# Kernel optimization log

Measured on AMD Instinct MI355X. Metric: run time of the kernel, lower is better.

The kernel has to match this reference:

```python
import jax, jax.numpy as jnp
import numpy as np

COMMITMENT_COST = 0.25


def setup_inputs() -> dict:
    key = jax.random.key(0)
    k1, k2 = jax.random.split(key)
    B, D, H, W = 16, 256, 32, 32
    K = 8192
    z = jax.random.normal(k1, (B, D, H, W), dtype=jnp.float32)
    embeddings = jax.random.uniform(k2, (K, D), dtype=jnp.float32,
                                    minval=-1.0 / K, maxval=1.0 / K)
    return {"z": z, "embeddings": embeddings}


def reference(z, embeddings):
    B, D, H, W = z.shape
    # NCHW -> NHWC, flatten spatial+batch to code vectors [N, D]
    z_p = jnp.transpose(z, (0, 2, 3, 1))
    z_flat = z_p.reshape(-1, D)
    # squared-distance via matmul: ||z||^2 + ||e||^2 - 2 z.e^T  -> [N, K]
    d = (jnp.sum(z_flat * z_flat, axis=1, keepdims=True)
         + jnp.sum(embeddings * embeddings, axis=1)
         - 2.0 * jnp.matmul(z_flat, embeddings.T))
    encoding_indices = jnp.argmin(d, axis=1)  # [N]
    quantized = embeddings[encoding_indices].reshape(z_p.shape)  # [B,H,W,D]
    e_latent_loss = jnp.mean((jax.lax.stop_gradient(quantized) - z_p) ** 2)
    q_latent_loss = jnp.mean((quantized - jax.lax.stop_gradient(z_p)) ** 2)
    loss = q_latent_loss + COMMITMENT_COST * e_latent_loss
    # straight-through estimator
    quantized_st = z_p + jax.lax.stop_gradient(quantized - z_p)
    out = jnp.transpose(quantized_st, (0, 3, 1, 2))  # back to NCHW
    return out, loss, encoding_indices.reshape(B, H, W)
```

## Files before the change

kernel.cpp:

```cpp
#include <hip/hip_runtime.h>

#define B_    16
#define D_    256
#define H_    32
#define W_    32
#define SP    1024
#define N_TOT 16384
#define K_    8192
#define ZB    (D_*SP)

#define BIAS_  0.03125f
#define DELTA_ 2.5e-4f

typedef __attribute__((ext_vector_type(8))) short bf16x8;
typedef __attribute__((ext_vector_type(4))) short bf16x4;
typedef __attribute__((ext_vector_type(4))) float f32x4;

#define GLOAD_LDS16(g, l) \
    __builtin_amdgcn_global_load_lds((const __attribute__((address_space(1))) void*)(g), \
                                     (__attribute__((address_space(3))) void*)(l), 16, 0, 0)

__device__ __forceinline__ unsigned short f2bf(float f) {
    unsigned u = __float_as_uint(f);
    u += 0x7FFFu + ((u >> 16) & 1u);
    return (unsigned short)(u >> 16);
}

__device__ __forceinline__ void merge2(unsigned &a1, unsigned &a2,
                                       unsigned b1, unsigned b2) {
    unsigned m1  = min(a1, b1);
    unsigned hi  = max(a1, b1);
    unsigned sel = (a1 < b1) ? a2 : b2;
    a2 = min(hi, sel);
    a1 = m1;
}


__global__ __launch_bounds__(256)
void cvt_e_enorm(const float* __restrict__ emb, short* __restrict__ ET3,
                 float* __restrict__ enorm, float* __restrict__ enormB) {
    int t = threadIdx.x;
    int k = blockIdx.x * 4 + (t >> 6);
    int l = t & 63;
    float4 v = *(const float4*)(emb + (size_t)k * D_ + l * 4);
    float sum = v.x*v.x + v.y*v.y + v.z*v.z + v.w*v.w;
    for (int m = 1; m < 64; m <<= 1) sum += __shfl_xor(sum, m, 64);
    if (l == 0) { enorm[k] = sum; enormB[k] = sum + BIAS_; }
    int dcb  = l >> 4;
    int c    = (l >> 1) & 7;
    int half = l & 1;
    bf16x4 o;
    o[0] = (short)f2bf(v.x); o[1] = (short)f2bf(v.y);
    o[2] = (short)f2bf(v.z); o[3] = (short)f2bf(v.w);
    *(bf16x4*)(ET3 + ((size_t)dcb * K_ + k) * 64 + ((c ^ (k & 7)) * 8) + half * 4) = o;
}


__global__ __launch_bounds__(256)
void zpart_cvtz(const float* __restrict__ z, float* __restrict__ zpart,
                short* __restrict__ ZT3) {
    int bx  = blockIdx.x;
    int dcb = bx >> 6;
    int st  = bx & 63;
    int t   = threadIdx.x;
    int n   = st * 256 + t;
    int b   = n >> 10;
    int s   = n & 1023;
    const float* zb = z + (size_t)b * ZB + (size_t)(dcb * 64) * SP + s;
    short* dst = ZT3 + ((size_t)dcb * N_TOT + n) * 64;
    int sw = n & 7;
#pragma unroll
    for (int c2 = 0; c2 < 4; ++c2) {
        float vv[16];
#pragma unroll
        for (int dd = 0; dd < 16; ++dd)
            vv[dd] = zb[(size_t)(c2 * 16 + dd) * SP];
        float sum = 0.f;
#pragma unroll
        for (int dd = 0; dd < 16; ++dd) {
            float v = vv[dd];
            sum += v * v;
        }
        zpart[(size_t)(dcb * 4 + c2) * N_TOT + n] = sum;
        bf16x8 o0, o1;
#pragma unroll
        for (int j = 0; j < 8; ++j) { o0[j] = (short)f2bf(vv[j]);
                                      o1[j] = (short)f2bf(vv[8 + j]); }
        *(bf16x8*)(dst + (((c2 * 2)     ^ sw) * 8)) = o0;
        *(bf16x8*)(dst + (((c2 * 2 + 1) ^ sw) * 8)) = o1;
    }
}

__global__ __launch_bounds__(256)
void znorm_kernel2(const float* __restrict__ zpart, float* __restrict__ znorm,
                   int* __restrict__ wl_cnt) {
    int n = blockIdx.x * 256 + threadIdx.x;
    float sum = 0.f;
#pragma unroll
    for (int dc = 0; dc < 16; ++dc) sum += zpart[(size_t)dc * N_TOT + n];
    znorm[n] = sum;
    if (n == 0) *wl_cnt = 0;
}


__global__ __launch_bounds__(256, 4)
void mfma_argmin2(const short* __restrict__ ET3, const short* __restrict__ ZT3,
                  const float* __restrict__ enormB, uint2* __restrict__ pv) {
    __shared__ char smem[32768];
    const int t    = threadIdx.x;
    const int wid  = t >> 6, lane = t & 63;
    const int quad = lane >> 4, l16 = lane & 15;
    const int wm   = wid >> 1, wn = wid & 1;
    const int stripe = blockIdx.x >> 7;
    const int n0     = (blockIdx.x & 127) * 128;
    const int swz    = (l16 & 7);

    unsigned r1[4], r2[4];
#pragma unroll
    for (int fj = 0; fj < 4; ++fj) { r1[fj] = 0xFFFFFFFFu; r2[fj] = 0xFFFFFFFFu; }

#pragma unroll 1
    for (int cc = 0; cc < 8; ++cc) {
        const int c0 = stripe * 1024 + cc * 128;
        f32x4 acc[4][4];
#pragma unroll
        for (int fi = 0; fi < 4; ++fi)
#pragma unroll
            for (int fj = 0; fj < 4; ++fj) acc[fi][fj] = (f32x4){0.f, 0.f, 0.f, 0.f};

#pragma unroll 1
        for (int dcb = 0; dcb < 4; ++dcb) {
            __syncthreads();
            const char* gA = (const char*)ET3 + ((size_t)dcb * K_    + c0) * 128;
            const char* gB = (const char*)ZT3 + ((size_t)dcb * N_TOT + n0) * 128;
#pragma unroll
            for (int j = 0; j < 4; ++j) {
                int off = j * 4096 + t * 16;
                GLOAD_LDS16(gA + off, smem + off);
                GLOAD_LDS16(gB + off, smem + 16384 + off);
            }
            __syncthreads();
#pragma unroll
            for (int dc2 = 0; dc2 < 2; ++dc2) {
                bf16x8 af[4], bfv[4];
                const int ch = ((dc2 * 4 + quad) ^ swz) * 16;
#pragma unroll
                for (int fi = 0; fi < 4; ++fi)
                    af[fi] = *(const bf16x8*)(smem + (wm*64 + fi*16 + l16)*128 + ch);
#pragma unroll
                for (int fj = 0; fj < 4; ++fj)
                    bfv[fj] = *(const bf16x8*)(smem + 16384 + (wn*64 + fj*16 + l16)*128 + ch);
#pragma unroll
                for (int fi = 0; fi < 4; ++fi)
#pragma unroll
                    for (int fj = 0; fj < 4; ++fj)
                        acc[fi][fj] = __builtin_amdgcn_mfma_f32_16x16x32_bf16(
                            af[fi], bfv[fj], acc[fi][fj], 0, 0, 0);
            }
        }

        float ekv[4][4];
#pragma unroll
        for (int fi = 0; fi < 4; ++fi) {
            float4 e4 = *(const float4*)(enormB + c0 + wm*64 + fi*16 + quad*4);
            ekv[fi][0]=e4.x; ekv[fi][1]=e4.y; ekv[fi][2]=e4.z; ekv[fi][3]=e4.w;
        }
#pragma unroll
        for (int fj = 0; fj < 4; ++fj) {
#pragma unroll
            for (int fi = 0; fi < 4; ++fi) {
                const unsigned cb = (unsigned)(c0 + wm*64 + fi*16 + quad*4);
                unsigned k0, k1, k2, k3;
                {
                    float s0 = fmaf(-2.f, acc[fi][fj].x, ekv[fi][0]);
                    float s1 = fmaf(-2.f, acc[fi][fj].y, ekv[fi][1]);
                    float s2 = fmaf(-2.f, acc[fi][fj].z, ekv[fi][2]);
                    float s3 = fmaf(-2.f, acc[fi][fj].w, ekv[fi][3]);
                    k0 = (__float_as_uint(s0) & 0xFFFFE000u) | (cb + 0u);
                    k1 = (__float_as_uint(s1) & 0xFFFFE000u) | (cb + 1u);
                    k2 = (__float_as_uint(s2) & 0xFFFFE000u) | (cb + 2u);
                    k3 = (__float_as_uint(s3) & 0xFFFFE000u) | (cb + 3u);
                }
                unsigned lo1 = min(k0, k1), hi1 = max(k0, k1);
                unsigned lo2 = min(k2, k3), hi2 = max(k2, k3);
                merge2(lo1, hi1, lo2, hi2);
                merge2(r1[fj], r2[fj], lo1, hi1);
            }
        }
    }

#pragma unroll
    for (int fj = 0; fj < 4; ++fj) {
        unsigned a1 = r1[fj], a2 = r2[fj];
#pragma unroll
        for (int m = 16; m <= 32; m <<= 1) {
            unsigned b1 = __shfl_xor(a1, m, 64);
            unsigned b2 = __shfl_xor(a2, m, 64);
            merge2(a1, a2, b1, b2);
        }
        if (quad == 0) {
            int n = n0 + wn*64 + fj*16 + l16;
            pv[(size_t)(stripe * 2 + wm) * N_TOT + n] = make_uint2(a1, a2);
        }
    }
}


__global__ __launch_bounds__(256)
void reduce_phaseA(const uint2* __restrict__ pv, int* __restrict__ fidx,
                   float* __restrict__ out_idx, int* __restrict__ wl,
                   int* __restrict__ wl_cnt, float* __restrict__ out_loss) {
    int n = blockIdx.x * 256 + threadIdx.x;
    if (n == 0) *out_loss = 0.f;
    uint2 pp[16];
    unsigned mn = 0xFFFFFFFFu;
#pragma unroll
    for (int g = 0; g < 16; ++g) {
        pp[g] = pv[(size_t)g * N_TOT + n];
        mn = min(mn, pp[g].x);
    }
    float smin  = __uint_as_float(mn & 0xFFFFE000u);
    unsigned th = __float_as_uint(smin + DELTA_) | 8191u;
    int cnt = 0;
#pragma unroll
    for (int g = 0; g < 16; ++g) {
        cnt += (pp[g].x <= th) ? 1 : 0;
        cnt += (pp[g].y <= th) ? 1 : 0;
    }
    if (cnt > 1) {
        int slot = atomicAdd(wl_cnt, 1);
        wl[slot] = n;
    } else {
        int c = (int)(mn & 8191u);
        fidx[n] = c;
        out_idx[n] = (float)c;
    }
}


__global__ __launch_bounds__(256)
void recheck_kernel(const uint2* __restrict__ pv, const float* __restrict__ znorm,
                    const float* __restrict__ enorm, const float* __restrict__ z,
                    const float* __restrict__ emb, const int* __restrict__ wl,
                    const int* __restrict__ wl_cnt, int* __restrict__ fidx,
                    float* __restrict__ out_idx) {
    __shared__ float zrow[4][256];
    const int lane = threadIdx.x & 63;
    const int wslot = threadIdx.x >> 6;
    const int gwave = (blockIdx.x * 256 + threadIdx.x) >> 6;
    const int nwaves = (gridDim.x * 256) >> 6;
    const int total = *wl_cnt;

    for (int i = gwave; i < total; i += nwaves) {
        int n = wl[i];
        unsigned key = 0xFFFFFFFFu;
        if (lane < 32) {
            uint2 p = pv[(size_t)(lane & 15) * N_TOT + n];
            key = (lane < 16) ? p.x : p.y;
        }
        unsigned mn = key;
#pragma unroll
        for (int m = 1; m < 64; m <<= 1) mn = min(mn, __shfl_xor(mn, m, 64));
        float smin  = __uint_as_float(mn & 0xFFFFE000u);
        unsigned th = __float_as_uint(smin + DELTA_) | 8191u;

        const int b = n >> 10, sp = n & 1023;
        const float* zr = z + (size_t)b * ZB + sp;
#pragma unroll
        for (int j = 0; j < 4; ++j)
            zrow[wslot][lane + j * 64] = zr[(size_t)(lane + j * 64) * SP];
        float zn = znorm[n];

        unsigned lexlo = 0xFFFFFFFFu, lexhi = 0xFFFFFFFFu;
        if (key <= th) {
            int c = (int)(key & 8191u);
            const float* er = emb + (size_t)c * D_;
            float dot = 0.f;
#pragma unroll 8
            for (int d = 0; d < D_; ++d)
                dot = fmaf(zrow[wslot][d], er[d], dot);
            float s = (zn + enorm[c]) - 2.f * dot;
            unsigned sb = __float_as_uint(s);
            lexhi = sb >> 19;
            lexlo = (sb << 13) | (unsigned)c;
        }
#pragma unroll
        for (int m = 1; m < 64; m <<= 1) {
            unsigned olo = __shfl_xor(lexlo, m, 64);
            unsigned ohi = __shfl_xor(lexhi, m, 64);
            if (ohi < lexhi || (ohi == lexhi && olo < lexlo)) { lexhi = ohi; lexlo = olo; }
        }
        if (lane == 0) {
            int c = (int)(lexlo & 8191u);
            fidx[n] = c;
            out_idx[n] = (float)c;
        }
    }
}


__global__ __launch_bounds__(256)
void output_kernel2(const float* __restrict__ z, const float* __restrict__ emb,
                    const int* __restrict__ fidx, float* __restrict__ out,
                    float* __restrict__ loss) {
    __shared__ float eL[32][257];
    __shared__ int   fid[32];
    __shared__ float red[4];
    const int nb = blockIdx.x;
    const int n0 = nb * 32;
    const int b  = n0 >> 10;
    const int s0 = n0 & 1023;
    const int t  = threadIdx.x;
    if (t < 32) fid[t] = fidx[n0 + t];
    __syncthreads();
#pragma unroll
    for (int i = 0; i < 8; ++i) {
        int p = t + i * 256;
        int row = p >> 6, q = p & 63;
        float4 v = *(const float4*)(emb + (size_t)fid[row] * D_ + q * 4);
        eL[row][q*4+0] = v.x; eL[row][q*4+1] = v.y;
        eL[row][q*4+2] = v.z; eL[row][q*4+3] = v.w;
    }
    __syncthreads();
    const int sl = t & 31, dg = t >> 5;
    float lsum = 0.f;
#pragma unroll
    for (int i = 0; i < 32; ++i) {
        int d = dg * 32 + i;
        size_t off = ((size_t)(b * D_ + d)) * SP + s0 + sl;
        float zv = z[off];
        float q  = eL[sl][d];
        float diff = q - zv;
        out[off] = zv + diff;
        lsum += diff * diff;
    }
    for (int m = 1; m < 64; m <<= 1) lsum += __shfl_xor(lsum, m, 64);
    if ((t & 63) == 0) red[t >> 6] = lsum;
    __syncthreads();
    if (t == 0) {
        float tot = (red[0] + red[1] + red[2] + red[3])
                    * (1.25f / (float)(B_ * SP * D_));
        atomicAdd(loss, tot);
    }
}

#define MT 128
#define CT 128
#define DT 32
#define NSTRIPE 8
#define CPS (K_/NSTRIPE)
#define ES (CT+4)

__global__ __launch_bounds__(256)
void enorm_kernel(const float* __restrict__ emb, float* __restrict__ enorm,
                  float* __restrict__ enormB) {
    int t = threadIdx.x;
    int k = blockIdx.x * 4 + (t >> 6);
    int l = t & 63;
    float4 v = *(const float4*)(emb + (size_t)k * D_ + l * 4);
    float sum = v.x*v.x + v.y*v.y + v.z*v.z + v.w*v.w;
    for (int m = 1; m < 64; m <<= 1) sum += __shfl_xor(sum, m, 64);
    if (l == 0) { enorm[k] = sum; enormB[k] = sum + BIAS_; }
}

__global__ __launch_bounds__(256)
void zpart_kernel(const float* __restrict__ z, float* __restrict__ zpart) {
    int bx = blockIdx.x;
    int b  = bx >> 4;
    int dc = bx & 15;
    int t  = threadIdx.x;
#pragma unroll
    for (int i = 0; i < 4; ++i) {
        int s = t + i * 256;
        float sum = 0.f;
#pragma unroll
        for (int dd = 0; dd < 16; ++dd) {
            float v = z[(size_t)b * ZB + (size_t)(dc * 16 + dd) * SP + s];
            sum += v * v;
        }
        zpart[(size_t)dc * N_TOT + b * SP + s] = sum;
    }
}

__global__ __launch_bounds__(256)
void znorm_kernel(const float* __restrict__ zpart, float* __restrict__ znorm) {
    int n = blockIdx.x * 256 + threadIdx.x;
    float sum = 0.f;
#pragma unroll
    for (int dc = 0; dc < 16; ++dc) sum += zpart[(size_t)dc * N_TOT + n];
    znorm[n] = sum;
}

__global__ __launch_bounds__(256)
void gemm_argmin(const float* __restrict__ z, const float* __restrict__ emb,
                 const float* __restrict__ enorm, const float* __restrict__ znorm,
                 float* __restrict__ pvals, int* __restrict__ pidx) {
    __shared__ float zsm[DT][MT];
    __shared__ float esm[DT][ES];
    const int t = threadIdx.x;
    const int bx = blockIdx.x;
    const int stripe = bx & (NSTRIPE - 1);
    const int rb = bx >> 3;
    const int n0 = rb * MT;
    const int b  = n0 / SP;
    const int s0 = n0 % SP;
    const float* zb = z + (size_t)b * ZB + s0;
    const int tc = t & 15;
    const int tr = t >> 4;
    float zn[8];
#pragma unroll
    for (int i = 0; i < 8; ++i) zn[i] = znorm[n0 + tr * 8 + i];
    float best[8]; int bidx[8];
#pragma unroll
    for (int i = 0; i < 8; ++i) { best[i] = 3.4e38f; bidx[i] = 0; }
    for (int cc = 0; cc < CPS / CT; ++cc) {
        const int c0 = stripe * CPS + cc * CT;
        float acc[8][8];
#pragma unroll
        for (int i = 0; i < 8; ++i)
#pragma unroll
            for (int j = 0; j < 8; ++j) acc[i][j] = 0.f;
        for (int dc = 0; dc < D_ / DT; ++dc) {
            const int d0 = dc * DT;
            __syncthreads();
#pragma unroll
            for (int i = 0; i < 4; ++i) {
                int p  = t + i * 256;
                int d  = p >> 5;
                int rq = p & 31;
                float4 v = *(const float4*)(zb + (size_t)(d0 + d) * SP + rq * 4);
                *(float4*)&zsm[d][rq * 4] = v;
            }
#pragma unroll
            for (int i = 0; i < 4; ++i) {
                int p  = t + i * 256;
                int c  = p >> 3;
                int dq = p & 7;
                float4 v = *(const float4*)(emb + (size_t)(c0 + c) * D_ + d0 + dq * 4);
                esm[dq * 4 + 0][c] = v.x;
                esm[dq * 4 + 1][c] = v.y;
                esm[dq * 4 + 2][c] = v.z;
                esm[dq * 4 + 3][c] = v.w;
            }
            __syncthreads();
#pragma unroll 8
            for (int d = 0; d < DT; ++d) {
                float zr[8], ec[8];
                *(float4*)&zr[0] = *(const float4*)&zsm[d][tr * 8];
                *(float4*)&zr[4] = *(const float4*)&zsm[d][tr * 8 + 4];
                *(float4*)&ec[0] = *(const float4*)&esm[d][tc * 8];
                *(float4*)&ec[4] = *(const float4*)&esm[d][tc * 8 + 4];
#pragma unroll
                for (int i = 0; i < 8; ++i)
#pragma unroll
                    for (int j = 0; j < 8; ++j)
                        acc[i][j] = fmaf(zr[i], ec[j], acc[i][j]);
            }
        }
        float ek[8];
#pragma unroll
        for (int j = 0; j < 8; ++j) ek[j] = enorm[c0 + tc * 8 + j];
#pragma unroll
        for (int i = 0; i < 8; ++i) {
#pragma unroll
            for (int j = 0; j < 8; ++j) {
                float s = (zn[i] + ek[j]) - 2.0f * acc[i][j];
                int code = c0 + tc * 8 + j;
                if (s < best[i] || (s == best[i] && code < bidx[i])) {
                    best[i] = s; bidx[i] = code;
                }
            }
        }
    }
#pragma unroll
    for (int i = 0; i < 8; ++i) {
        float v = best[i]; int ix = bidx[i];
        for (int m = 1; m < 16; m <<= 1) {
            float ov = __shfl_xor(v, m, 64);
            int   oi = __shfl_xor(ix, m, 64);
            if (ov < v || (ov == v && oi < ix)) { v = ov; ix = oi; }
        }
        if (tc == 0) {
            int n = n0 + tr * 8 + i;
            pvals[n * NSTRIPE + stripe] = v;
            pidx [n * NSTRIPE + stripe] = ix;
        }
    }
}

__global__ __launch_bounds__(256)
void reduce_rows(const float* __restrict__ pvals, const int* __restrict__ pidx,
                 int* __restrict__ fidx, float* __restrict__ out_idx) {
    int n = blockIdx.x * 256 + threadIdx.x;
    float bv = 3.4e38f; int bi = 0;
#pragma unroll
    for (int s = 0; s < NSTRIPE; ++s) {
        float v = pvals[n * NSTRIPE + s];
        int  ix = pidx [n * NSTRIPE + s];
        if (v < bv || (v == bv && ix < bi)) { bv = v; bi = ix; }
    }
    fidx[n] = bi;
    out_idx[n] = (float)bi;
}


extern "C" void kernel_launch(void* const* d_in, const int* in_sizes, int n_in,
                              void* d_out, int out_size, void* d_ws, size_t ws_size,
                              hipStream_t stream) {
    const float* z   = (const float*)d_in[0];
    const float* emb = (const float*)d_in[1];
    float* out = (float*)d_out;
    float* w   = (float*)d_ws;

    float* enorm  = w;
    float* enormB = w + 8192;
    float* znorm  = w + 16384;
    int*   fidx   = (int*)(w + 32768);

    float* out0     = out;
    float* out_loss = out + (size_t)B_ * D_ * SP;
    float* out_idx  = out_loss + 1;

    const size_t NEED = 3735680ULL * 4ULL;
    if (ws_size >= NEED) {
        int*   wl_cnt = (int*)(w + 49152);
        int*   wl     = (int*)(w + 49216);
        uint2* pv     = (uint2*)(w + 65664);
        float* zpart  = w + 65664;
        short* ET3    = (short*)(w + 589952);
        short* ZT3    = (short*)(w + 1638528);

        cvt_e_enorm<<<K_ / 4, 256, 0, stream>>>(emb, ET3, enorm, enormB);
        zpart_cvtz<<<256, 256, 0, stream>>>(z, zpart, ZT3);
        znorm_kernel2<<<N_TOT / 256, 256, 0, stream>>>(zpart, znorm, wl_cnt);
        mfma_argmin2<<<1024, 256, 0, stream>>>(ET3, ZT3, enormB, pv);
        reduce_phaseA<<<N_TOT / 256, 256, 0, stream>>>(pv, fidx, out_idx, wl,
                                                       wl_cnt, out_loss);
        recheck_kernel<<<256, 256, 0, stream>>>(pv, znorm, enorm, z, emb,
                                                wl, wl_cnt, fidx, out_idx);
        output_kernel2<<<N_TOT / 32, 256, 0, stream>>>(z, emb, fidx, out0, out_loss);
    } else {
        float* zpart = w + 32768;
        float* znF   = w + 294912;
        float* pvals = w + 311296;
        int*   pidxF = (int*)(w + 442368);
        int*   fidxF = (int*)(w + 573440);
        fidx = fidxF;
        enorm_kernel<<<K_ / 4, 256, 0, stream>>>(emb, enorm, enormB);
        zpart_kernel<<<B_ * 16, 256, 0, stream>>>(z, zpart);
        znorm_kernel<<<N_TOT / 256, 256, 0, stream>>>(zpart, znF);
        gemm_argmin<<<(N_TOT / MT) * NSTRIPE, 256, 0, stream>>>(z, emb, enorm, znF,
                                                                pvals, pidxF);
        reduce_rows<<<N_TOT / 256, 256, 0, stream>>>(pvals, pidxF, fidx, out_idx);
        hipMemsetAsync(out_loss, 0, sizeof(float), stream);
        output_kernel2<<<N_TOT / 32, 256, 0, stream>>>(z, emb, fidx, out0, out_loss);
    }
}
```

Measured before the change: 230.7 us.

## Add 256x256-tile double-buffered MFMA argmin kernel with row-major bf16 operands

After: 248.5 us. +7.7%, slower.

```diff
diff --git a/kernel.cpp b/kernel.cpp
--- a/kernel.cpp
+++ b/kernel.cpp
@@ -33,6 +33,266 @@
     unsigned sel = (a1 < b1) ? a2 : b2;
     a2 = min(hi, sel);
     a1 = m1;
+}
+
+
+__global__ __launch_bounds__(256)
+void cvt_e_enorm_p(const float* __restrict__ emb, short* __restrict__ ET,
+                   float* __restrict__ enorm, float* __restrict__ enormB) {
+    int t = threadIdx.x;
+    int k = blockIdx.x * 4 + (t >> 6);
+    int l = t & 63;
+    float4 v = *(const float4*)(emb + (size_t)k * D_ + l * 4);
+    float sum = v.x*v.x + v.y*v.y + v.z*v.z + v.w*v.w;
+    for (int m = 1; m < 64; m <<= 1) sum += __shfl_xor(sum, m, 64);
+    if (l == 0) { enorm[k] = sum; enormB[k] = sum + BIAS_; }
+    bf16x4 o;
+    o[0] = (short)f2bf(v.x); o[1] = (short)f2bf(v.y);
+    o[2] = (short)f2bf(v.z); o[3] = (short)f2bf(v.w);
+    *(bf16x4*)(ET + (size_t)k * D_ + l * 4) = o;
+}
+
+__global__ __launch_bounds__(256)
+void zpart_cvtz_p(const float* __restrict__ z, float* __restrict__ zpart,
+                  short* __restrict__ ZT) {
+    int bx  = blockIdx.x;
+    int dcb = bx >> 6;
+    int st  = bx & 63;
+    int t   = threadIdx.x;
+    int n   = st * 256 + t;
+    int b   = n >> 10;
+    int s   = n & 1023;
+    const float* zb = z + (size_t)b * ZB + (size_t)(dcb * 64) * SP + s;
+    short* dst = ZT + (size_t)n * D_ + dcb * 64;
+#pragma unroll
+    for (int c2 = 0; c2 < 4; ++c2) {
+        float vv[16];
+#pragma unroll
+        for (int dd = 0; dd < 16; ++dd)
+            vv[dd] = zb[(size_t)(c2 * 16 + dd) * SP];
+        float sum = 0.f;
+#pragma unroll
+        for (int dd = 0; dd < 16; ++dd) {
+            float v = vv[dd];
+            sum += v * v;
+        }
+        zpart[(size_t)(dcb * 4 + c2) * N_TOT + n] = sum;
+        bf16x8 o0, o1;
+#pragma unroll
+        for (int j = 0; j < 8; ++j) { o0[j] = (short)f2bf(vv[j]);
+                                      o1[j] = (short)f2bf(vv[8 + j]); }
+        *(bf16x8*)(dst + c2 * 16)     = o0;
+        *(bf16x8*)(dst + c2 * 16 + 8) = o1;
+    }
+}
+
+__device__ __forceinline__ int stg_off(int base_row, int idx) {
+    int r  = idx >> 2;
+    int lc = (idx & 3) ^ ((r >> 1) & 3);
+    return (base_row + r) * 256 + lc * 8;
+}
+
+__global__ __launch_bounds__(512, 2)
+void mfma_argmin3(const short* __restrict__ ET, const short* __restrict__ ZT,
+                  const float* __restrict__ enormB, uint2* __restrict__ pv) {
+    __shared__ char smem[65536];
+    const int t    = threadIdx.x;
+    const int wid  = t >> 6, lane = t & 63;
+    const int quad = lane >> 4, l16 = lane & 15;
+    const int wm   = wid & 3, wn = wid >> 2;
+    const int cb     = blockIdx.x & 31;
+    const int rb     = blockIdx.x >> 5;
+    const int c_base = cb * 256, n_base = rb * 256;
+
+    const int offA0 = stg_off(c_base, t);
+    const int offA1 = stg_off(c_base, t + 512);
+    const int offB0 = stg_off(n_base, t);
+    const int offB1 = stg_off(n_base, t + 512);
+
+#define ISSUE_STAGE(dcb, h) { \
+    char* As_ = smem + (h) * 32768; \
+    char* Bs_ = As_ + 16384; \
+    GLOAD_LDS16(ET + offA0 + (dcb) * 32, As_ + t * 16); \
+    GLOAD_LDS16(ET + offA1 + (dcb) * 32, As_ + 8192 + t * 16); \
+    GLOAD_LDS16(ZT + offB0 + (dcb) * 32, Bs_ + t * 16); \
+    GLOAD_LDS16(ZT + offB1 + (dcb) * 32, Bs_ + 8192 + t * 16); }
+
+    f32x4 acc[4][8];
+#pragma unroll
+    for (int fi = 0; fi < 4; ++fi)
+#pragma unroll
+        for (int fj = 0; fj < 8; ++fj) acc[fi][fj] = (f32x4){0.f, 0.f, 0.f, 0.f};
+
+    const int ch = (quad ^ ((l16 >> 1) & 3)) * 16;
+    ISSUE_STAGE(0, 0);
+    __syncthreads();
+#pragma unroll 1
+    for (int s = 0; s < 8; ++s) {
+        if (s < 7) ISSUE_STAGE(s + 1, (s + 1) & 1);
+        const char* As = smem + (s & 1) * 32768;
+        const char* Bs = As + 16384;
+        bf16x8 a[4];
+#pragma unroll
+        for (int fi = 0; fi < 4; ++fi)
+            a[fi] = *(const bf16x8*)(As + (wm * 64 + fi * 16 + l16) * 64 + ch);
+#pragma unroll
+        for (int fj = 0; fj < 8; ++fj) {
+            bf16x8 bv = *(const bf16x8*)(Bs + (wn * 128 + fj * 16 + l16) * 64 + ch);
+#pragma unroll
+            for (int fi = 0; fi < 4; ++fi)
+                acc[fi][fj] = __builtin_amdgcn_mfma_f32_16x16x32_bf16(
+                    a[fi], bv, acc[fi][fj], 0, 0, 0);
+        }
+        __syncthreads();
+    }
+#undef ISSUE_STAGE
+
+    unsigned r1[8], r2[8];
+#pragma unroll
+    for (int fj = 0; fj < 8; ++fj) { r1[fj] = 0xFFFFFFFFu; r2[fj] = 0xFFFFFFFFu; }
+    float ekv[4][4];
+#pragma unroll
+    for (int fi = 0; fi < 4; ++fi) {
+        float4 e4 = *(const float4*)(enormB + c_base + wm * 64 + fi * 16 + quad * 4);
+        ekv[fi][0]=e4.x; ekv[fi][1]=e4.y; ekv[fi][2]=e4.z; ekv[fi][3]=e4.w;
+    }
+#pragma unroll
+    for (int fj = 0; fj < 8; ++fj) {
+#pragma unroll
+        for (int fi = 0; fi < 4; ++fi) {
+            const unsigned cbs = (unsigned)(c_base + wm * 64 + fi * 16 + quad * 4);
+            float s0 = fmaf(-2.f, acc[fi][fj].x, ekv[fi][0]);
+            float s1 = fmaf(-2.f, acc[fi][fj].y, ekv[fi][1]);
+            float s2 = fmaf(-2.f, acc[fi][fj].z, ekv[fi][2]);
+            float s3 = fmaf(-2.f, acc[fi][fj].w, ekv[fi][3]);
+            unsigned k0 = (__float_as_uint(s0) & 0xFFFFE000u) | (cbs + 0u);
+            unsigned k1 = (__float_as_uint(s1) & 0xFFFFE000u) | (cbs + 1u);
+            unsigned k2 = (__float_as_uint(s2) & 0xFFFFE000u) | (cbs + 2u);
+            unsigned k3 = (__float_as_uint(s3) & 0xFFFFE000u) | (cbs + 3u);
+            unsigned lo1 = min(k0, k1), hi1 = max(k0, k1);
+            unsigned lo2 = min(k2, k3), hi2 = max(k2, k3);
+            merge2(lo1, hi1, lo2, hi2);
+            merge2(r1[fj], r2[fj], lo1, hi1);
+        }
+    }
+    uint2* mbuf = (uint2*)smem;
+#pragma unroll
+    for (int fj = 0; fj < 8; ++fj) {
+        unsigned a1 = r1[fj], a2 = r2[fj];
+#pragma unroll
+        for (int m = 16; m <= 32; m <<= 1) {
+            unsigned b1 = __shfl_xor(a1, m, 64);
+            unsigned b2 = __shfl_xor(a2, m, 64);
+            merge2(a1, a2, b1, b2);
+        }
+        if (quad == 0)
+            mbuf[wm * 256 + wn * 128 + fj * 16 + l16] = make_uint2(a1, a2);
+    }
+    __syncthreads();
+    if (t < 256) {
+        uint2 P = mbuf[t];
+        unsigned a1 = P.x, a2 = P.y;
+#pragma unroll
+        for (int g = 1; g < 4; ++g) {
+            uint2 Q = mbuf[g * 256 + t];
+            merge2(a1, a2, Q.x, Q.y);
+        }
+        pv[(size_t)cb * N_TOT + n_base + t] = make_uint2(a1, a2);
+    }
+}
+
+
+template <int NG>
+__global__ __launch_bounds__(256)
+void reduce_phaseA_t(const uint2* __restrict__ pv, int* __restrict__ fidx,
+                     float* __restrict__ out_idx, int* __restrict__ wl,
+                     int* __restrict__ wl_cnt, float* __restrict__ out_loss) {
+    int n = blockIdx.x * 256 + threadIdx.x;
+    if (n == 0) *out_loss = 0.f;
+    uint2 pp[NG];
+    unsigned mn = 0xFFFFFFFFu;
+#pragma unroll
+    for (int g = 0; g < NG; ++g) {
+        pp[g] = pv[(size_t)g * N_TOT + n];
+        mn = min(mn, pp[g].x);
+    }
+    float smin  = __uint_as_float(mn & 0xFFFFE000u);
+    unsigned th = __float_as_uint(smin + DELTA_) | 8191u;
+    int cnt = 0;
+#pragma unroll
+    for (int g = 0; g < NG; ++g) {
+        cnt += (pp[g].x <= th) ? 1 : 0;
+        cnt += (pp[g].y <= th) ? 1 : 0;
+    }
+    if (cnt > 1) {
+        int slot = atomicAdd(wl_cnt, 1);
+        wl[slot] = n;
+    } else {
+        int c = (int)(mn & 8191u);
+        fidx[n] = c;
+        out_idx[n] = (float)c;
+    }
+}
+
+template <int NG>
+__global__ __launch_bounds__(256)
+void recheck_t(const uint2* __restrict__ pv, const float* __restrict__ znorm,
+               const float* __restrict__ enorm, const float* __restrict__ z,
+               const float* __restrict__ emb, const int* __restrict__ wl,
+               const int* __restrict__ wl_cnt, int* __restrict__ fidx,
+               float* __restrict__ out_idx) {
+    __shared__ float zrow[4][256];
+    const int lane = threadIdx.x & 63;
+    const int wslot = threadIdx.x >> 6;
+    const int gwave = (blockIdx.x * 256 + threadIdx.x) >> 6;
+    const int nwaves = (gridDim.x * 256) >> 6;
+    const int total = *wl_cnt;
+
+    for (int i = gwave; i < total; i += nwaves) {
+        int n = wl[i];
+        unsigned key = 0xFFFFFFFFu;
+        if (lane < 2 * NG) {
+            uint2 p = pv[(size_t)(lane >> 1) * N_TOT + n];
+            key = (lane & 1) ? p.y : p.x;
+        }
+        unsigned mn = key;
+#pragma unroll
+        for (int m = 1; m < 64; m <<= 1) mn = min(mn, __shfl_xor(mn, m, 64));
+        float smin  = __uint_as_float(mn & 0xFFFFE000u);
+        unsigned th = __float_as_uint(smin + DELTA_) | 8191u;
+
+        const int b = n >> 10, sp = n & 1023;
+        const float* zr = z + (size_t)b * ZB + sp;
+#pragma unroll
+        for (int j = 0; j < 4; ++j)
+            zrow[wslot][lane + j * 64] = zr[(size_t)(lane + j * 64) * SP];
+        float zn = znorm[n];
+
+        unsigned lexlo = 0xFFFFFFFFu, lexhi = 0xFFFFFFFFu;
+        if (key <= th) {
+            int c = (int)(key & 8191u);
+            const float* er = emb + (size_t)c * D_;
+            float dot = 0.f;
+#pragma unroll 8
+            for (int d = 0; d < D_; ++d)
+                dot = fmaf(zrow[wslot][d], er[d], dot);
+            float s = (zn + enorm[c]) - 2.f * dot;
+            unsigned sb = __float_as_uint(s);
+            lexhi = sb >> 19;
+            lexlo = (sb << 13) | (unsigned)c;
+        }
+#pragma unroll
+        for (int m = 1; m < 64; m <<= 1) {
+            unsigned olo = __shfl_xor(lexlo, m, 64);
+            unsigned ohi = __shfl_xor(lexhi, m, 64);
+            if (ohi < lexhi || (ohi == lexhi && olo < lexlo)) { lexhi = ohi; lexlo = olo; }
+        }
+        if (lane == 0) {
+            int c = (int)(lexlo & 8191u);
+            fidx[n] = c;
+            out_idx[n] = (float)c;
+        }
+    }
 }
 
 
@@ -55,7 +315,6 @@
     *(bf16x4*)(ET3 + ((size_t)dcb * K_ + k) * 64 + ((c ^ (k & 7)) * 8) + half * 4) = o;
 }
 
-
 __global__ __launch_bounds__(256)
 void zpart_cvtz(const float* __restrict__ z, float* __restrict__ zpart,
                 short* __restrict__ ZT3) {
@@ -91,18 +350,6 @@
     }
 }
 
-__global__ __launch_bounds__(256)
-void znorm_kernel2(const float* __restrict__ zpart, float* __restrict__ znorm,
-                   int* __restrict__ wl_cnt) {
-    int n = blockIdx.x * 256 + threadIdx.x;
-    float sum = 0.f;
-#pragma unroll
-    for (int dc = 0; dc < 16; ++dc) sum += zpart[(size_t)dc * N_TOT + n];
-    znorm[n] = sum;
-    if (n == 0) *wl_cnt = 0;
-}
-
-
 __global__ __launch_bounds__(256, 4)
 void mfma_argmin2(const short* __restrict__ ET3, const short* __restrict__ ZT3,
                   const float* __restrict__ enormB, uint2* __restrict__ pv) {
@@ -143,13 +390,13 @@
 #pragma unroll
             for (int dc2 = 0; dc2 < 2; ++dc2) {
                 bf16x8 af[4], bfv[4];
-                const int ch = ((dc2 * 4 + quad) ^ swz) * 16;
+                const int chm = ((dc2 * 4 + quad) ^ swz) * 16;
 #pragma unroll
                 for (int fi = 0; fi < 4; ++fi)
-                    af[fi] = *(const bf16x8*)(smem + (wm*64 + fi*16 + l16)*128 + ch);
+                    af[fi] = *(const bf16x8*)(smem + (wm*64 + fi*16 + l16)*128 + chm);
 #pragma unroll
                 for (int fj = 0; fj < 4; ++fj)
-                    bfv[fj] = *(const bf16x8*)(smem + 16384 + (wn*64 + fj*16 + l16)*128 + ch);
+                    bfv[fj] = *(const bf16x8*)(smem + 16384 + (wn*64 + fj*16 + l16)*128 + chm);
 #pragma unroll
                 for (int fi = 0; fi < 4; ++fi)
 #pragma unroll
@@ -170,17 +417,14 @@
 #pragma unroll
             for (int fi = 0; fi < 4; ++fi) {
                 const unsigned cb = (unsigned)(c0 + wm*64 + fi*16 + quad*4);
-                unsigned k0, k1, k2, k3;
-                {
-                    float s0 = fmaf(-2.f, acc[fi][fj].x, ekv[fi][0]);
-                    float s1 = fmaf(-2.f, acc[fi][fj].y, ekv[fi][1]);
-                    float s2 = fmaf(-2.f, acc[fi][fj].z, ekv[fi][2]);
-                    float s3 = fmaf(-2.f, acc[fi][fj].w, ekv[fi][3]);
-                    k0 = (__float_as_uint(s0) & 0xFFFFE000u) | (cb + 0u);
-                    k1 = (__float_as_uint(s1) & 0xFFFFE000u) | (cb + 1u);
-                    k2 = (__float_as_uint(s2) & 0xFFFFE000u) | (cb + 2u);
-                    k3 = (__float_as_uint(s3) & 0xFFFFE000u) | (cb + 3u);
-                }
+                float s0 = fmaf(-2.f, acc[fi][fj].x, ekv[fi][0]);
+                float s1 = fmaf(-2.f, acc[fi][fj].y, ekv[fi][1]);
+                float s2 = fmaf(-2.f, acc[fi][fj].z, ekv[fi][2]);
+                float s3 = fmaf(-2.f, acc[fi][fj].w, ekv[fi][3]);
+                unsigned k0 = (__float_as_uint(s0) & 0xFFFFE000u) | (cb + 0u);
+                unsigned k1 = (__float_as_uint(s1) & 0xFFFFE000u) | (cb + 1u);
+                unsigned k2 = (__float_as_uint(s2) & 0xFFFFE000u) | (cb + 2u);
+                unsigned k3 = (__float_as_uint(s3) & 0xFFFFE000u) | (cb + 3u);
                 unsigned lo1 = min(k0, k1), hi1 = max(k0, k1);
                 unsigned lo2 = min(k2, k3), hi2 = max(k2, k3);
                 merge2(lo1, hi1, lo2, hi2);
@@ -207,97 +451,15 @@
 
 
 __global__ __launch_bounds__(256)
-void reduce_phaseA(const uint2* __restrict__ pv, int* __restrict__ fidx,
-                   float* __restrict__ out_idx, int* __restrict__ wl,
-                   int* __restrict__ wl_cnt, float* __restrict__ out_loss) {
+void znorm_kernel2(const float* __restrict__ zpart, float* __restrict__ znorm,
+                   int* __restrict__ wl_cnt) {
     int n = blockIdx.x * 256 + threadIdx.x;
-    if (n == 0) *out_loss = 0.f;
-    uint2 pp[16];
-    unsigned mn = 0xFFFFFFFFu;
-#pragma unroll
-    for (int g = 0; g < 16; ++g) {
-        pp[g] = pv[(size_t)g * N_TOT + n];
-        mn = min(mn, pp[g].x);
-    }
-    float smin  = __uint_as_float(mn & 0xFFFFE000u);
-    unsigned th = __float_as_uint(smin + DELTA_) | 8191u;
-    int cnt = 0;
-#pragma unroll
-    for (int g = 0; g < 16; ++g) {
-        cnt += (pp[g].x <= th) ? 1 : 0;
-        cnt += (pp[g].y <= th) ? 1 : 0;
-    }
-    if (cnt > 1) {
-        int slot = atomicAdd(wl_cnt, 1);
-        wl[slot] = n;
-    } else {
-        int c = (int)(mn & 8191u);
-        fidx[n] = c;
-        out_idx[n] = (float)c;
-    }
-}
-
-
-__global__ __launch_bounds__(256)
-void recheck_kernel(const uint2* __restrict__ pv, const float* __restrict__ znorm,
-                    const float* __restrict__ enorm, const float* __restrict__ z,
-                    const float* __restrict__ emb, const int* __restrict__ wl,
-                    const int* __restrict__ wl_cnt, int* __restrict__ fidx,
-                    float* __restrict__ out_idx) {
-    __shared__ float zrow[4][256];
-    const int lane = threadIdx.x & 63;
-    const int wslot = threadIdx.x >> 6;
-    const int gwave = (blockIdx.x * 256 + threadIdx.x) >> 6;
-    const int nwaves = (gridDim.x * 256) >> 6;
-    const int total = *wl_cnt;
-
-    for (int i = gwave; i < total; i += nwaves) {
-        int n = wl[i];
-        unsigned key = 0xFFFFFFFFu;
-        if (lane < 32) {
-            uint2 p = pv[(size_t)(lane & 15) * N_TOT + n];
-            key = (lane < 16) ? p.x : p.y;
-        }
-        unsigned mn = key;
-#pragma unroll
-        for (int m = 1; m < 64; m <<= 1) mn = min(mn, __shfl_xor(mn, m, 64));
-        float smin  = __uint_as_float(mn & 0xFFFFE000u);
-        unsigned th = __float_as_uint(smin + DELTA_) | 8191u;
-
-        const int b = n >> 10, sp = n & 1023;
-        const float* zr = z + (size_t)b * ZB + sp;
-#pragma unroll
-        for (int j = 0; j < 4; ++j)
-            zrow[wslot][lane + j * 64] = zr[(size_t)(lane + j * 64) * SP];
-        float zn = znorm[n];
-
-        unsigned lexlo = 0xFFFFFFFFu, lexhi = 0xFFFFFFFFu;
-        if (key <= th) {
-            int c = (int)(key & 8191u);
-            const float* er = emb + (size_t)c * D_;
-            float dot = 0.f;
-#pragma unroll 8
-            for (int d = 0; d < D_; ++d)
-                dot = fmaf(zrow[wslot][d], er[d], dot);
-            float s = (zn + enorm[c]) - 2.f * dot;
-            unsigned sb = __float_as_uint(s);
-            lexhi = sb >> 19;
-            lexlo = (sb << 13) | (unsigned)c;
-        }
-#pragma unroll
-        for (int m = 1; m < 64; m <<= 1) {
-            unsigned olo = __shfl_xor(lexlo, m, 64);
-            unsigned ohi = __shfl_xor(lexhi, m, 64);
-            if (ohi < lexhi || (ohi == lexhi && olo < lexlo)) { lexhi = ohi; lexlo = olo; }
-        }
-        if (lane == 0) {
-            int c = (int)(lexlo & 8191u);
-            fidx[n] = c;
-            out_idx[n] = (float)c;
-        }
-    }
-}
-
+    float sum = 0.f;
+#pragma unroll
+    for (int dc = 0; dc < 16; ++dc) sum += zpart[(size_t)dc * N_TOT + n];
+    znorm[n] = sum;
+    if (n == 0) *wl_cnt = 0;
+}
 
 __global__ __launch_bounds__(256)
 void output_kernel2(const float* __restrict__ z, const float* __restrict__ emb,
@@ -344,165 +506,6 @@
     }
 }
 
-#define MT 128
-#define CT 128
-#define DT 32
-#define NSTRIPE 8
-#define CPS (K_/NSTRIPE)
-#define ES (CT+4)
-
-__global__ __launch_bounds__(256)
-void enorm_kernel(const float* __restrict__ emb, float* __restrict__ enorm,
-                  float* __restrict__ enormB) {
-    int t = threadIdx.x;
-    int k = blockIdx.x * 4 + (t >> 6);
-    int l = t & 63;
-    float4 v = *(const float4*)(emb + (size_t)k * D_ + l * 4);
-    float sum = v.x*v.x + v.y*v.y + v.z*v.z + v.w*v.w;
-    for (int m = 1; m < 64; m <<= 1) sum += __shfl_xor(sum, m, 64);
-    if (l == 0) { enorm[k] = sum; enormB[k] = sum + BIAS_; }
-}
-
-__global__ __launch_bounds__(256)
-void zpart_kernel(const float* __restrict__ z, float* __restrict__ zpart) {
-    int bx = blockIdx.x;
-    int b  = bx >> 4;
-    int dc = bx & 15;
-    int t  = threadIdx.x;
-#pragma unroll
-    for (int i = 0; i < 4; ++i) {
-        int s = t + i * 256;
-        float sum = 0.f;
-#pragma unroll
-        for (int dd = 0; dd < 16; ++dd) {
-            float v = z[(size_t)b * ZB + (size_t)(dc * 16 + dd) * SP + s];
-            sum += v * v;
-        }
-        zpart[(size_t)dc * N_TOT + b * SP + s] = sum;
-    }
-}
-
-__global__ __launch_bounds__(256)
-void znorm_kernel(const float* __restrict__ zpart, float* __restrict__ znorm) {
-    int n = blockIdx.x * 256 + threadIdx.x;
-    float sum = 0.f;
-#pragma unroll
-    for (int dc = 0; dc < 16; ++dc) sum += zpart[(size_t)dc * N_TOT + n];
-    znorm[n] = sum;
-}
-
-__global__ __launch_bounds__(256)
-void gemm_argmin(const float* __restrict__ z, const float* __restrict__ emb,
-                 const float* __restrict__ enorm, const float* __restrict__ znorm,
-                 float* __restrict__ pvals, int* __restrict__ pidx) {
-    __shared__ float zsm[DT][MT];
-    __shared__ float esm[DT][ES];
-    const int t = threadIdx.x;
-    const int bx = blockIdx.x;
-    const int stripe = bx & (NSTRIPE - 1);
-    const int rb = bx >> 3;
-    const int n0 = rb * MT;
-    const int b  = n0 / SP;
-    const int s0 = n0 % SP;
-    const float* zb = z + (size_t)b * ZB + s0;
-    const int tc = t & 15;
-    const int tr = t >> 4;
-    float zn[8];
-#pragma unroll
-    for (int i = 0; i < 8; ++i) zn[i] = znorm[n0 + tr * 8 + i];
-    float best[8]; int bidx[8];
-#pragma unroll
-    for (int i = 0; i < 8; ++i) { best[i] = 3.4e38f; bidx[i] = 0; }
-    for (int cc = 0; cc < CPS / CT; ++cc) {
-        const int c0 = stripe * CPS + cc * CT;
-        float acc[8][8];
-#pragma unroll
-        for (int i = 0; i < 8; ++i)
-#pragma unroll
-            for (int j = 0; j < 8; ++j) acc[i][j] = 0.f;
-        for (int dc = 0; dc < D_ / DT; ++dc) {
-            const int d0 = dc * DT;
-            __syncthreads();
-#pragma unroll
-            for (int i = 0; i < 4; ++i) {
-                int p  = t + i * 256;
-                int d  = p >> 5;
-                int rq = p & 31;
-                float4 v = *(const float4*)(zb + (size_t)(d0 + d) * SP + rq * 4);
-                *(float4*)&zsm[d][rq * 4] = v;
-            }
-#pragma unroll
-            for (int i = 0; i < 4; ++i) {
-                int p  = t + i * 256;
-                int c  = p >> 3;
-                int dq = p & 7;
-                float4 v = *(const float4*)(emb + (size_t)(c0 + c) * D_ + d0 + dq * 4);
-                esm[dq * 4 + 0][c] = v.x;
-                esm[dq * 4 + 1][c] = v.y;
-                esm[dq * 4 + 2][c] = v.z;
-                esm[dq * 4 + 3][c] = v.w;
-            }
-            __syncthreads();
-#pragma unroll 8
-            for (int d = 0; d < DT; ++d) {
-                float zr[8], ec[8];
-                *(float4*)&zr[0] = *(const float4*)&zsm[d][tr * 8];
-                *(float4*)&zr[4] = *(const float4*)&zsm[d][tr * 8 + 4];
-                *(float4*)&ec[0] = *(const float4*)&esm[d][tc * 8];
-                *(float4*)&ec[4] = *(const float4*)&esm[d][tc * 8 + 4];
-#pragma unroll
-                for (int i = 0; i < 8; ++i)
-#pragma unroll
-                    for (int j = 0; j < 8; ++j)
-                        acc[i][j] = fmaf(zr[i], ec[j], acc[i][j]);
-            }
-        }
-        float ek[8];
-#pragma unroll
-        for (int j = 0; j < 8; ++j) ek[j] = enorm[c0 + tc * 8 + j];
-#pragma unroll
-        for (int i = 0; i < 8; ++i) {
-#pragma unroll
-            for (int j = 0; j < 8; ++j) {
-                float s = (zn[i] + ek[j]) - 2.0f * acc[i][j];
-                int code = c0 + tc * 8 + j;
-                if (s < best[i] || (s == best[i] && code < bidx[i])) {
-                    best[i] = s; bidx[i] = code;
-                }
-            }
-        }
-    }
-#pragma unroll
-    for (int i = 0; i < 8; ++i) {
-        float v = best[i]; int ix = bidx[i];
-        for (int m = 1; m < 16; m <<= 1) {
-            float ov = __shfl_xor(v, m, 64);
-            int   oi = __shfl_xor(ix, m, 64);
-            if (ov < v || (ov == v && oi < ix)) { v = ov; ix = oi; }
-        }
-        if (tc == 0) {
-            int n = n0 + tr * 8 + i;
-            pvals[n * NSTRIPE + stripe] = v;
-            pidx [n * NSTRIPE + stripe] = ix;
-        }
-    }
-}
-
-__global__ __launch_bounds__(256)
-void reduce_rows(const float* __restrict__ pvals, const int* __restrict__ pidx,
-                 int* __restrict__ fidx, float* __restrict__ out_idx) {
-    int n = blockIdx.x * 256 + threadIdx.x;
-    float bv = 3.4e38f; int bi = 0;
-#pragma unroll
-    for (int s = 0; s < NSTRIPE; ++s) {
-        float v = pvals[n * NSTRIPE + s];
-        int  ix = pidx [n * NSTRIPE + s];
-        if (v < bv || (v == bv && ix < bi)) { bv = v; bi = ix; }
-    }
-    fidx[n] = bi;
-    out_idx[n] = (float)bi;
-}
-
 
 extern "C" void kernel_launch(void* const* d_in, const int* in_sizes, int n_in,
                               void* d_out, int out_size, void* d_ws, size_t ws_size,
@@ -516,43 +519,42 @@
     float* enormB = w + 8192;
     float* znorm  = w + 16384;
     int*   fidx   = (int*)(w + 32768);
+    int*   wl_cnt = (int*)(w + 49152);
+    int*   wl     = (int*)(w + 49216);
 
     float* out0     = out;
     float* out_loss = out + (size_t)B_ * D_ * SP;
     float* out_idx  = out_loss + 1;
 
-    const size_t NEED = 3735680ULL * 4ULL;
-    if (ws_size >= NEED) {
-        int*   wl_cnt = (int*)(w + 49152);
-        int*   wl     = (int*)(w + 49216);
-        uint2* pv     = (uint2*)(w + 65664);
-        float* zpart  = w + 65664;
-        short* ET3    = (short*)(w + 589952);
-        short* ZT3    = (short*)(w + 1638528);
+    const size_t NEED_BIG = 4259968ULL * 4ULL;
+    if (ws_size >= NEED_BIG) {
+        uint2* pv    = (uint2*)(w + 65664);
+        float* zpart = w + 65664;
+        short* ET    = (short*)(w + 1114240);
+        short* ZT    = (short*)(w + 2162816);
+
+        cvt_e_enorm_p<<<K_ / 4, 256, 0, stream>>>(emb, ET, enorm, enormB);
+        zpart_cvtz_p<<<256, 256, 0, stream>>>(z, zpart, ZT);
+        znorm_kernel2<<<N_TOT / 256, 256, 0, stream>>>(zpart, znorm, wl_cnt);
+        mfma_argmin3<<<2048, 512, 0, stream>>>(ET, ZT, enormB, pv);
+        reduce_phaseA_t<32><<<N_TOT / 256, 256, 0, stream>>>(pv, fidx, out_idx,
+                                                             wl, wl_cnt, out_loss);
+        recheck_t<32><<<256, 256, 0, stream>>>(pv, znorm, enorm, z, emb,
+                                               wl, wl_cnt, fidx, out_idx);
+    } else {
+        uint2* pv    = (uint2*)(w + 65664);
+        float* zpart = w + 65664;
+        short* ET3   = (short*)(w + 589952);
+        short* ZT3   = (short*)(w + 1638528);
 
         cvt_e_enorm<<<K_ / 4, 256, 0, stream>>>(emb, ET3, enorm, enormB);
         zpart_cvtz<<<256, 256, 0, stream>>>(z, zpart, ZT3);
         znorm_kernel2<<<N_TOT / 256, 256, 0, stream>>>(zpart, znorm, wl_cnt);
         mfma_argmin2<<<1024, 256, 0, stream>>>(ET3, ZT3, enormB, pv);
-        reduce_phaseA<<<N_TOT / 256, 256, 0, stream>>>(pv, fidx, out_idx, wl,
-                                                       wl_cnt, out_loss);
-        recheck_kernel<<<256, 256, 0, stream>>>(pv, znorm, enorm, z, emb,
-                                                wl, wl_cnt, fidx, out_idx);
-        output_kernel2<<<N_TOT / 32, 256, 0, stream>>>(z, emb, fidx, out0, out_loss);
-    } else {
-        float* zpart = w + 32768;
-        float* znF   = w + 294912;
-        float* pvals = w + 311296;
-        int*   pidxF = (int*)(w + 442368);
-        int*   fidxF = (int*)(w + 573440);
-        fidx = fidxF;
-        enorm_kernel<<<K_ / 4, 256, 0, stream>>>(emb, enorm, enormB);
-        zpart_kernel<<<B_ * 16, 256, 0, stream>>>(z, zpart);
-        znorm_kernel<<<N_TOT / 256, 256, 0, stream>>>(zpart, znF);
-        gemm_argmin<<<(N_TOT / MT) * NSTRIPE, 256, 0, stream>>>(z, emb, enorm, znF,
-                                                                pvals, pidxF);
-        reduce_rows<<<N_TOT / 256, 256, 0, stream>>>(pvals, pidxF, fidx, out_idx);
-        hipMemsetAsync(out_loss, 0, sizeof(float), stream);
-        output_kernel2<<<N_TOT / 32, 256, 0, stream>>>(z, emb, fidx, out0, out_loss);
-    }
-}
+        reduce_phaseA_t<16><<<N_TOT / 256, 256, 0, stream>>>(pv, fidx, out_idx,
+                                                             wl, wl_cnt, out_loss);
+        recheck_t<16><<<256, 256, 0, stream>>>(pv, znorm, enorm, z, emb,
+                                               wl, wl_cnt, fidx, out_idx);
+    }
+    output_kernel2<<<N_TOT / 32, 256, 0, stream>>>(z, emb, fidx, out0, out_loss);
+}
```
